# Kernel optimization log

Hardware: AMD Instinct MI355X
Metric: run time of the kernel (lower is better)

Reference implementation:

```python
import jax, jax.numpy as jnp
import numpy as np

N_HEAD, N_KV_HEAD, HEAD_DIM = 16, 4, 128
EPS = 1e-5


def rms_norm(x, eps=EPS):
    return x * jax.lax.rsqrt(jnp.mean(x * x, axis=-1, keepdims=True) + eps)


def apply_rope(x, cos, sin):
    # x: (B,T,H,D); cos/sin: (1,T,1,D//2)
    d = x.shape[-1] // 2
    x1, x2 = x[..., :d], x[..., d:]
    return jnp.concatenate([x1 * cos - x2 * sin, x1 * sin + x2 * cos], axis=-1)


def setup_inputs() -> dict:
    key = jax.random.key(0)
    ks = jax.random.split(key, 6)
    B, T, C = 4, 2048, 2048
    H, KV, D = N_HEAD, N_KV_HEAD, HEAD_DIM
    x = jax.random.normal(ks[0], (B, T, C), dtype=jnp.float32)
    # RoPE tables (llama-style, theta=10000)
    inv_freq = 1.0 / (10000.0 ** (jnp.arange(D // 2, dtype=jnp.float32) / (D // 2)))
    ang = jnp.arange(T, dtype=jnp.float32)[:, None] * inv_freq[None, :]  # (T, D/2)
    cos = jnp.cos(ang)[None, :, None, :]
    sin = jnp.sin(ang)[None, :, None, :]
    s = 0.02
    wq = jax.random.normal(ks[1], (C, H * D), dtype=jnp.float32) * s
    wk = jax.random.normal(ks[2], (C, KV * D), dtype=jnp.float32) * s
    wv = jax.random.normal(ks[3], (C, KV * D), dtype=jnp.float32) * s
    wproj = jax.random.normal(ks[4], (H * D, C), dtype=jnp.float32) * s
    return {"x": x, "cos": cos, "sin": sin, "wq": wq, "wk": wk, "wv": wv, "wproj": wproj}


def reference(x, cos, sin, wq, wk, wv, wproj):
    B, T, C = x.shape
    H, KV, D = N_HEAD, N_KV_HEAD, HEAD_DIM
    n_rep = H // KV
    q = (x @ wq).reshape(B, T, H, D)
    k = (x @ wk).reshape(B, T, KV, D)
    v = (x @ wv).reshape(B, T, KV, D)
    q = apply_rope(q, cos, sin)
    k = apply_rope(k, cos, sin)
    # QK-norm (use_qk_norm=True)
    q = rms_norm(q)
    k = rms_norm(k)
    # GQA: expand kv heads (matches torch repeat_interleave on head dim)
    k = jnp.repeat(k, n_rep, axis=2)
    v = jnp.repeat(v, n_rep, axis=2)
    scale = 1.0 / np.sqrt(D).astype(np.float32)
    scores = jnp.einsum('bqhd,bkhd->bhqk', q, k) * scale  # (B,H,T,T)
    causal = jnp.tril(jnp.ones((T, T), dtype=bool))
    scores = jnp.where(causal[None, None], scores, jnp.finfo(scores.dtype).min)
    p = jax.nn.softmax(scores, axis=-1)
    y = jnp.einsum('bhqk,bkhd->bqhd', p, v).reshape(B, T, H * D)
    return y @ wproj
```

## Files before the change

kernel.cpp:

```cpp
#include <hip/hip_runtime.h>
#include <hip/hip_bf16.h>
#include <stdint.h>

using bf16 = __hip_bfloat16;
typedef __attribute__((ext_vector_type(8))) short short8;
typedef __attribute__((ext_vector_type(4))) float f32x4;
typedef __attribute__((ext_vector_type(16))) float f32x16;

#define MFMA16(a,b,c) __builtin_amdgcn_mfma_f32_16x16x32_bf16(a,b,c,0,0,0)
#define MFMA32(a,b,c) __builtin_amdgcn_mfma_f32_32x32x16_bf16(a,b,c,0,0,0)

__device__ __forceinline__ void gload_lds16(const void* g, void* l) {
  __builtin_amdgcn_global_load_lds((const __attribute__((address_space(1))) void*)g,
                                   (__attribute__((address_space(3))) void*)l, 16, 0, 0);
}

__device__ __forceinline__ short bf_bits(float f) {
  bf16 h = __float2bfloat16(f);
  return *reinterpret_cast<short*>(&h);
}
__device__ __forceinline__ unsigned int pk2(float a, float b) {
  unsigned int r;
  asm("v_cvt_pk_bf16_f32 %0, %1, %2" : "=v"(r) : "v"(a), "v"(b));
  return r;
}
__device__ __forceinline__ float bf2f(short s) {
  return __uint_as_float((unsigned int)(unsigned short)s << 16);
}
__device__ __forceinline__ float exp2g(float x) { return __builtin_amdgcn_exp2f(x); }

__global__ __launch_bounds__(256) void f32_to_bf16_k(const float* __restrict__ in,
                                                     bf16* __restrict__ out, size_t n) {
  size_t i = ((size_t)blockIdx.x * 256 + threadIdx.x) * 8;
  if (i >= n) return;
  float4 a = *(const float4*)(in + i);
  float4 b = *(const float4*)(in + i + 4);
  short8 pk;
  pk[0] = bf_bits(a.x); pk[1] = bf_bits(a.y); pk[2] = bf_bits(a.z); pk[3] = bf_bits(a.w);
  pk[4] = bf_bits(b.x); pk[5] = bf_bits(b.y); pk[6] = bf_bits(b.z); pk[7] = bf_bits(b.w);
  *(short8*)(out + i) = pk;
}

__global__ __launch_bounds__(256) void transpose_cvt_k(const float* __restrict__ in,
                                                       bf16* __restrict__ out, int K, int N) {
  __shared__ float tile[32][33];
  int n0 = blockIdx.x * 32, k0 = blockIdx.y * 32;
  int tx = threadIdx.x & 31, ty = threadIdx.x >> 5;
#pragma unroll
  for (int j = 0; j < 4; ++j) {
    int kk = ty + j * 8;
    tile[kk][tx] = in[(size_t)(k0 + kk) * N + n0 + tx];
  }
  __syncthreads();
#pragma unroll
  for (int j = 0; j < 4; ++j) {
    int nn = ty + j * 8;
    out[(size_t)(n0 + nn) * K + k0 + tx] = __float2bfloat16(tile[tx][nn]);
  }
}

__global__ __launch_bounds__(256) void transpose_v_k(const bf16* __restrict__ qkv,
                                                     bf16* __restrict__ vt) {
  constexpr int T = 2048, Dh = 128, KV = 4, QKVW = 3072, VOFF = 2560;
  __shared__ bf16 tile[32][33];
  int t0 = blockIdx.x * 32, d0 = blockIdx.y * 32;
  int b = blockIdx.z >> 2, kv = blockIdx.z & 3;
  int tx = threadIdx.x & 31, ty = threadIdx.x >> 5;
#pragma unroll
  for (int j = 0; j < 4; ++j) {
    int tt = ty + j * 8;
    tile[tt][tx] = qkv[((size_t)(b * T + t0 + tt)) * QKVW + VOFF + kv * Dh + d0 + tx];
  }
  __syncthreads();
#pragma unroll
  for (int j = 0; j < 4; ++j) {
    int dd = ty + j * 8;
    vt[((size_t)((b * KV + kv) * Dh + d0 + dd)) * T + t0 + tx] = tile[tx][dd];
  }
}

__global__ __launch_bounds__(256) void rope_rms_k(bf16* __restrict__ buf, int rowstride,
                                                  int baseoff,
                                                  const float* __restrict__ cosp,
                                                  const float* __restrict__ sinp,
                                                  int nh, float outscale) {
  constexpr int T = 2048;
  int wid = blockIdx.x * 4 + (threadIdx.x >> 6);
  int lane = threadIdx.x & 63;
  int h = wid % nh;
  int tok = wid / nh;
  int t = tok & (T - 1);
  bf16* p = buf + (size_t)tok * rowstride + baseoff + h * 128;
  float x1 = __bfloat162float(p[lane]);
  float x2 = __bfloat162float(p[lane + 64]);
  float c = cosp[t * 64 + lane], s = sinp[t * 64 + lane];
  float o1 = x1 * c - x2 * s;
  float o2 = x1 * s + x2 * c;
  float ss = o1 * o1 + o2 * o2;
#pragma unroll
  for (int m = 1; m < 64; m <<= 1) ss += __shfl_xor(ss, m, 64);
  float r = rsqrtf(ss * (1.f / 128.f) + 1e-5f) * outscale;
  p[lane] = __float2bfloat16(o1 * r);
  p[lane + 64] = __float2bfloat16(o2 * r);
}

#define PHASE(buf, i0, ...)                                                       \
  {                                                                               \
    short8 a00 = ldA(buf, i0, 0), a01 = ldA(buf, i0, 1);                          \
    short8 a10 = ldA(buf, (i0) + 1, 0), a11 = ldA(buf, (i0) + 1, 1);              \
    __VA_ARGS__;                                                                  \
    __builtin_amdgcn_s_barrier();                                                 \
    asm volatile("s_waitcnt lgkmcnt(0)" ::: "memory");                            \
    __builtin_amdgcn_s_setprio(1);                                                \
    _Pragma("unroll") for (int j = 0; j < 4; ++j) {                               \
      acc[i0][j] = MFMA16(a00, bf_[2 * j], acc[i0][j]);                           \
      acc[i0][j] = MFMA16(a01, bf_[2 * j + 1], acc[i0][j]);                       \
      acc[(i0) + 1][j] = MFMA16(a10, bf_[2 * j], acc[(i0) + 1][j]);               \
      acc[(i0) + 1][j] = MFMA16(a11, bf_[2 * j + 1], acc[(i0) + 1][j]);           \
    }                                                                             \
    __builtin_amdgcn_s_setprio(0);                                                \
  }
#define LOADB(buf)                                                                \
  _Pragma("unroll") for (int j = 0; j < 4; ++j) {                                 \
    bf_[2 * j] = ldB(buf, j, 0);                                                  \
    bf_[2 * j + 1] = ldB(buf, j, 1);                                              \
  }
#define BAR __builtin_amdgcn_s_barrier()

template <typename OutT>
__global__ __launch_bounds__(512, 2) void gemm256(const bf16* __restrict__ A,
                                                  const bf16* __restrict__ Bt,
                                                  OutT* __restrict__ C, int K,
                                                  int NT, int ldC) {
  __shared__ char lds[131072];
  const int tid = threadIdx.x, lane = tid & 63, w = tid >> 6;
  const int wm = w >> 2, wn = w & 3;
  const int bx = blockIdx.x;
  const int chunk = gridDim.x >> 3;
  const int wgid = (bx & 7) * chunk + (bx >> 3);
  const int m0 = (wgid / NT) * 256, n0 = (wgid % NT) * 256;
  const int lm = lane & 15;
  const int sw = (lane & 7) << 4;
  const int g16 = (lane >> 4) << 4;
  const size_t strideAB = (size_t)K * 2;

  auto stageA = [&](int buf, int h, int t) {
#pragma unroll
    for (int p2 = 0; p2 < 2; ++p2) {
      int off = tid * 16 + p2 * 8192;
      int row = off >> 7, cb = off & 127;
      int scb = cb ^ ((row & 7) << 4);
      gload_lds16((const char*)A + (size_t)(m0 + h * 128 + row) * strideAB + t * 128 + scb,
                  lds + buf * 65536 + h * 16384 + off);
    }
  };
  auto stageB = [&](int buf, int h, int t) {
#pragma unroll
    for (int p2 = 0; p2 < 2; ++p2) {
      int off = tid * 16 + p2 * 8192;
      int row = off >> 7, cb = off & 127;
      int scb = cb ^ ((row & 7) << 4);
      gload_lds16((const char*)Bt + (size_t)(n0 + h * 128 + row) * strideAB + t * 128 + scb,
                  lds + buf * 65536 + 32768 + h * 16384 + off);
    }
  };
  auto ldA = [&](int buf, int i, int ks) {
    int row = wm * 128 + i * 16 + lm;
    return *(const short8*)(lds + buf * 65536 + row * 128 + ((ks * 64 + g16) ^ sw));
  };
  auto ldB = [&](int buf, int j, int ks) {
    int row = wn * 64 + j * 16 + lm;
    return *(const short8*)(lds + buf * 65536 + 32768 + row * 128 + ((ks * 64 + g16) ^ sw));
  };

  f32x4 acc[8][4] = {};
  short8 bf_[8];
  const int niter = K / 128;

  stageA(0, 0, 0); stageA(0, 1, 0); stageB(0, 0, 0); stageB(0, 1, 0);
  stageB(1, 0, 1); stageB(1, 1, 1);
  asm volatile("s_waitcnt vmcnt(4)" ::: "memory");
  BAR;

  for (int i = 0; i < niter; ++i) {
    const int t0 = 2 * i, t1 = 2 * i + 1;
    const bool nl = (i + 1 < niter);
    LOADB(0);
    PHASE(0, 0, stageA(1, 0, t1)); BAR;
    PHASE(0, 2, stageA(1, 1, t1)); BAR;
    PHASE(0, 4, if (nl) stageB(0, 0, t0 + 2)); BAR;
    PHASE(0, 6, if (nl) stageB(0, 1, t0 + 2));
    if (nl) { asm volatile("s_waitcnt vmcnt(4)" ::: "memory"); }
    else    { asm volatile("s_waitcnt vmcnt(0)" ::: "memory"); }
    BAR;
    LOADB(1);
    PHASE(1, 0, if (nl) stageA(0, 0, t0 + 2)); BAR;
    PHASE(1, 2, if (nl) stageA(0, 1, t0 + 2)); BAR;
    PHASE(1, 4, if (nl) stageB(1, 0, t1 + 2)); BAR;
    PHASE(1, 6, if (nl) stageB(1, 1, t1 + 2));
    if (nl) { asm volatile("s_waitcnt vmcnt(4)" ::: "memory"); }
    BAR;
  }

  if constexpr (sizeof(OutT) == 2) {
    __syncthreads();
    bf16* sC = (bf16*)lds;
#pragma unroll
    for (int i = 0; i < 8; ++i) {
      int row = wm * 128 + i * 16 + (lane >> 4) * 4;
#pragma unroll
      for (int j = 0; j < 4; ++j) {
        int col = wn * 64 + j * 16 + lm;
#pragma unroll
        for (int r = 0; r < 4; ++r) sC[(row + r) * 256 + col] = __float2bfloat16(acc[i][j][r]);
      }
    }
    __syncthreads();
#pragma unroll
    for (int p = 0; p < 16; ++p) {
      int off = tid * 16 + p * 8192;
      int row = off >> 9, cb = off & 511;
      *(short8*)((char*)C + ((size_t)(m0 + row) * ldC + n0) * 2 + cb) =
          *(const short8*)(lds + off);
    }
  } else {
#pragma unroll
    for (int i = 0; i < 8; ++i) {
      int row = m0 + wm * 128 + i * 16 + (lane >> 4) * 4;
#pragma unroll
      for (int j = 0; j < 4; ++j) {
        int col = n0 + wn * 64 + j * 16 + lm;
#pragma unroll
        for (int r = 0; r < 4; ++r) C[(size_t)(row + r) * ldC + col] = acc[i][j][r];
      }
    }
  }
}

template <typename OutT>
__global__ __launch_bounds__(256) void gemm_bt(const bf16* __restrict__ A,
                                               const bf16* __restrict__ Bt,
                                               OutT* __restrict__ C, int K,
                                               int NT, int ldC) {
  constexpr int BM = 128, BN = 128, BK = 64;
  __shared__ char smem[32768];
  bf16* sA = (bf16*)smem;
  bf16* sB = (bf16*)(smem + 16384);
  int tid = threadIdx.x;
  int lane = tid & 63, w = tid >> 6;
  int flat = blockIdx.x;
  int wgid = (flat & 7) * (gridDim.x >> 3) + (flat >> 3);
  int m0 = (wgid / NT) * BM, n0 = (wgid % NT) * BN;
  int wm = (w >> 1) * 64, wn = (w & 1) * 64;
  f32x4 acc[4][4] = {};
  int nk = K / BK;
  for (int kt = 0; kt < nk; ++kt) {
    __syncthreads();
    int kb = kt * BK;
#pragma unroll
    for (int it = 0; it < 4; ++it) {
      int off = tid * 16 + it * 4096;
      int row = off >> 7, cb = off & 127;
      gload_lds16((const char*)A + (((size_t)(m0 + row)) * K + kb) * 2 + cb, (char*)sA + off);
    }
#pragma unroll
    for (int it = 0; it < 4; ++it) {
      int off = tid * 16 + it * 4096;
      int row = off >> 7, cb = off & 127;
      gload_lds16((const char*)Bt + (((size_t)(n0 + row)) * K + kb) * 2 + cb, (char*)sB + off);
    }
    asm volatile("s_waitcnt vmcnt(0)" ::: "memory");
    __syncthreads();
#pragma unroll
    for (int ks = 0; ks < 2; ++ks) {
      short8 af[4], bfr[4];
#pragma unroll
      for (int i = 0; i < 4; ++i) {
        af[i]  = *(const short8*)(sA + (wm + i * 16 + (lane & 15)) * BK + ks * 32 + (lane >> 4) * 8);
        bfr[i] = *(const short8*)(sB + (wn + i * 16 + (lane & 15)) * BK + ks * 32 + (lane >> 4) * 8);
      }
#pragma unroll
      for (int i = 0; i < 4; ++i)
#pragma unroll
        for (int j = 0; j < 4; ++j)
          acc[i][j] = MFMA16(af[i], bfr[j], acc[i][j]);
    }
  }
  if constexpr (sizeof(OutT) == 2) {
    __syncthreads();
    bf16* sC = (bf16*)smem;
#pragma unroll
    for (int i = 0; i < 4; ++i) {
      int row = wm + i * 16 + (lane >> 4) * 4;
#pragma unroll
      for (int j = 0; j < 4; ++j) {
        int col = wn + j * 16 + (lane & 15);
#pragma unroll
        for (int r = 0; r < 4; ++r)
          sC[(row + r) * BN + col] = __float2bfloat16(acc[i][j][r]);
      }
    }
    __syncthreads();
#pragma unroll
    for (int it = 0; it < 8; ++it) {
      int off = tid * 16 + it * 4096;
      int row = off >> 8, cb = off & 255;
      *(short8*)((char*)C + ((size_t)(m0 + row) * ldC + n0) * 2 + cb) =
          *(const short8*)(smem + off);
    }
  } else {
#pragma unroll
    for (int i = 0; i < 4; ++i) {
      int row = m0 + wm + i * 16 + (lane >> 4) * 4;
#pragma unroll
      for (int j = 0; j < 4; ++j) {
        int col = n0 + wn + j * 16 + (lane & 15);
#pragma unroll
        for (int r = 0; r < 4; ++r)
          C[(size_t)(row + r) * ldC + col] = acc[i][j][r];
      }
    }
  }
}

__global__ __launch_bounds__(512, 2) void attn_k(const bf16* __restrict__ qkv,
                                                 const bf16* __restrict__ vt,
                                                 bf16* __restrict__ y,
                                                 const float* __restrict__ cosp,
                                                 const float* __restrict__ sinp) {
  constexpr int T = 2048, Dh = 128, KV = 4, KB = 64, QKVW = 3072, KOFF = 2048;
  __shared__ char lds[65536];
  const int tid = threadIdx.x, lane = tid & 63, w = tid >> 6;
  const int hi = lane >> 5, lq = lane & 31;
  const int bx = blockIdx.x;
  const int idx = (bx >> 6) & 3;
  const int qt = (bx < 256) ? (7 - idx) : idx;
  const int b = (bx >> 4) & 3, h = bx & 15;
  const int kh = h >> 2;
  const int q0 = qt * 256 + w * 32;
  const int qg = q0 + lq;
  const int swz = (lane & 7) << 4;

  short8 aq[8];
  {
    const bf16* qp = qkv + ((size_t)(b * T + qg)) * QKVW + h * Dh + hi * 8;
#pragma unroll
    for (int m = 0; m < 8; ++m) aq[m] = *(const short8*)(qp + m * 16);
  }
  __builtin_amdgcn_s_waitcnt(0);

  {
    float ss = 0.f;
#pragma unroll
    for (int m = 0; m < 8; ++m)
#pragma unroll
      for (int e = 0; e < 8; ++e) { float v = bf2f(aq[m][e]); ss += v * v; }
    ss += __shfl_xor(ss, 32, 64);
    float rn = rsqrtf(ss * (1.f / 128.f) + 1e-5f) * (0.08838834764831845f * 1.4426950408889634f);
    const float4* cq4 = (const float4*)(cosp + (size_t)qg * 64) + hi * 2;
    const float4* sq4 = (const float4*)(sinp + (size_t)qg * 64) + hi * 2;
#pragma unroll
    for (int m = 0; m < 4; ++m) {
      float4 c0 = cq4[m * 4], c1 = cq4[m * 4 + 1];
      float4 s0 = sq4[m * 4], s1 = sq4[m * 4 + 1];
      float cc[8] = {c0.x, c0.y, c0.z, c0.w, c1.x, c1.y, c1.z, c1.w};
      float sn[8] = {s0.x, s0.y, s0.z, s0.w, s1.x, s1.y, s1.z, s1.w};
      short8 xl = aq[m], xh = aq[m + 4], nl, nh;
#pragma unroll
      for (int e = 0; e < 8; ++e) {
        float x1 = bf2f(xl[e]), x2 = bf2f(xh[e]);
        nl[e] = bf_bits((x1 * cc[e] - x2 * sn[e]) * rn);
        nh[e] = bf_bits((x1 * sn[e] + x2 * cc[e]) * rn);
      }
      aq[m] = nl; aq[m + 4] = nh;
    }
  }

  f32x16 acc[4] = {};
  float mrow = -1e4f, lrow = 0.f;

  auto stage = [&](int buf, int kv0) {
#pragma unroll
    for (int p = 0; p < 2; ++p) {
      int off = tid * 16 + p * 8192;
      int row = off >> 8, cb = off & 255;
      int scb = cb ^ ((row & 7) << 4);
      gload_lds16((const char*)qkv + (((size_t)(b * T + kv0 + row)) * QKVW + KOFF + kh * Dh) * 2 + scb,
                  lds + buf * 16384 + off);
    }
#pragma unroll
    for (int p = 0; p < 2; ++p) {
      int off = tid * 16 + p * 8192;
      int row = off >> 7, cb = off & 127;
      int scb = cb ^ ((row & 7) << 4);
      gload_lds16((const char*)vt + (((size_t)((b * KV + kh) * Dh + row)) * T + kv0) * 2 + scb,
                  lds + 32768 + buf * 16384 + off);
    }
  };

  const int nt = (qt + 1) * 4;
  const int lastit = (q0 + 31) >> 6;
  stage(0, 0);

  for (int it = 0; it < nt; ++it) {
    int cur = it & 1;
    if (it + 1 < nt) { stage(cur ^ 1, (it + 1) * KB); asm volatile("s_waitcnt vmcnt(4)" ::: "memory"); }
    else             { asm volatile("s_waitcnt vmcnt(0)" ::: "memory"); }
    __builtin_amdgcn_s_barrier();
    if (it <= lastit) {
      const char* sK = lds + cur * 16384;
      const char* sV = lds + 32768 + cur * 16384;
      const int kv0 = it * KB;

      f32x16 s0 = {}, s1 = {};
      __builtin_amdgcn_s_setprio(1);
#pragma unroll
      for (int m = 0; m < 8; ++m) {
        short8 ak = *(const short8*)(sK + lq * 256 + ((m * 32 + hi * 16) ^ swz));
        s0 = MFMA32(ak, aq[m], s0);
      }
#pragma unroll
      for (int m = 0; m < 8; ++m) {
        short8 ak = *(const short8*)(sK + (32 + lq) * 256 + ((m * 32 + hi * 16) ^ swz));
        s1 = MFMA32(ak, aq[m], s1);
      }
      __builtin_amdgcn_s_setprio(0);

      if (kv0 + 63 > q0) {
#pragma unroll
        for (int r = 0; r < 16; ++r) {
          int krow = (r & 3) + 8 * (r >> 2) + 4 * hi;
          if (kv0 + krow > qg) s0[r] = -1e30f;
          if (kv0 + 32 + krow > qg) s1[r] = -1e30f;
        }
      }

      float mx[16];
#pragma unroll
      for (int r = 0; r < 16; ++r) mx[r] = fmaxf(s0[r], s1[r]);
#pragma unroll
      for (int st = 8; st > 0; st >>= 1)
#pragma unroll
        for (int r = 0; r < 16; ++r) if (r < st) mx[r] = fmaxf(mx[r], mx[r + st]);
      float tmax = fmaxf(mx[0], __shfl_xor(mx[0], 32, 64));
      if (!__all(tmax - mrow <= 11.5f)) {
        float mn = fmaxf(mrow, tmax);
        float corr = exp2g(mrow - mn);
        mrow = mn;
        lrow *= corr;
#pragma unroll
        for (int dt = 0; dt < 4; ++dt)
#pragma unroll
          for (int r = 0; r < 16; ++r) acc[dt][r] *= corr;
      }
      float sm[16];
#pragma unroll
      for (int r = 0; r < 16; ++r) {
        s0[r] = exp2g(s0[r] - mrow);
        s1[r] = exp2g(s1[r] - mrow);
        sm[r] = s0[r] + s1[r];
      }
#pragma unroll
      for (int st = 8; st > 0; st >>= 1)
#pragma unroll
        for (int r = 0; r < 16; ++r) if (r < st) sm[r] += sm[r + st];
      lrow += sm[0] + __shfl_xor(sm[0], 32, 64);

      unsigned int u[16];
#pragma unroll
      for (int g = 0; g < 4; ++g) {
        u[g * 2 + 0] = pk2(s0[4 * g + 0], s0[4 * g + 1]);
        u[g * 2 + 1] = pk2(s0[4 * g + 2], s0[4 * g + 3]);
        u[8 + g * 2 + 0] = pk2(s1[4 * g + 0], s1[4 * g + 1]);
        u[8 + g * 2 + 1] = pk2(s1[4 * g + 2], s1[4 * g + 3]);
      }
      short8 pb[4];
#pragma unroll
      for (int kvs = 0; kvs < 4; ++kvs) {
        unsigned int lo0 = u[4 * kvs + 0], lo1 = u[4 * kvs + 1];
        unsigned int hi0 = u[4 * kvs + 2], hi1 = u[4 * kvs + 3];
        asm volatile("v_permlane32_swap_b32 %0, %1" : "+v"(lo0), "+v"(hi0));
        asm volatile("v_permlane32_swap_b32 %0, %1" : "+v"(lo1), "+v"(hi1));
        union { short8 v; unsigned int q[4]; } P;
        P.q[0] = lo0; P.q[1] = lo1; P.q[2] = hi0; P.q[3] = hi1;
        pb[kvs] = P.v;
      }

      __builtin_amdgcn_s_setprio(1);
#pragma unroll
      for (int dt = 0; dt < 4; ++dt) {
#pragma unroll
        for (int kvs = 0; kvs < 4; ++kvs) {
          short8 av = *(const short8*)(sV + (dt * 32 + lq) * 128 + ((kvs * 32 + hi * 16) ^ swz));
          acc[dt] = MFMA32(av, pb[kvs], acc[dt]);
        }
      }
      __builtin_amdgcn_s_setprio(0);
    }
    __builtin_amdgcn_s_barrier();
  }

  float inv = 1.f / lrow;
  __syncthreads();
  char* myO = lds + w * 8192;
#pragma unroll
  for (int dt = 0; dt < 4; ++dt)
#pragma unroll
    for (int i = 0; i < 8; ++i) {
      int d = ((2 * i) & 3) + 8 * (i >> 1) + 4 * hi;
      unsigned int pkd = pk2(acc[dt][2 * i] * inv, acc[dt][2 * i + 1] * inv);
      *(unsigned int*)(myO + lq * 256 + ((dt * 64 + d * 2) ^ ((lq & 7) << 4))) = pkd;
    }
  __syncthreads();
  const int row0 = b * T + qt * 256;
#pragma unroll
  for (int p = 0; p < 8; ++p) {
    int off = (p * 512 + tid) * 16;
    int q = off >> 8, cb = off & 255;
    short8 v = *(const short8*)(lds + (q >> 5) * 8192 + (q & 31) * 256 + (cb ^ ((q & 7) << 4)));
    *(short8*)((char*)y + ((size_t)(row0 + q) * 2048 + h * 128) * 2 + cb) = v;
  }
}

extern "C" void kernel_launch(void* const* d_in, const int* in_sizes, int n_in,
                              void* d_out, int out_size, void* d_ws, size_t ws_size,
                              hipStream_t stream) {
  const float* x    = (const float*)d_in[0];
  const float* cosp = (const float*)d_in[1];
  const float* sinp = (const float*)d_in[2];
  const float* wq   = (const float*)d_in[3];
  const float* wk   = (const float*)d_in[4];
  const float* wv   = (const float*)d_in[5];
  const float* wp   = (const float*)d_in[6];
  float* out = (float*)d_out;

  constexpr size_t Mtok = 8192;
  constexpr int Cdim = 2048, HD = 2048, KVD = 512, QKVW = 3072;

  char* ws = (char*)d_ws;
  bf16* xb    = (bf16*)ws; ws += Mtok * Cdim * 2;
  bf16* wqkvT = (bf16*)ws; ws += (size_t)QKVW * Cdim * 2;
  bf16* wpT   = (bf16*)ws; ws += (size_t)Cdim * HD * 2;
  bf16* qkv   = (bf16*)ws; ws += Mtok * QKVW * 2;
  bf16* vtb   = (bf16*)ws; ws += Mtok * KVD * 2;
  bf16* yb    = (bf16*)ws; ws += Mtok * HD * 2;

  f32_to_bf16_k<<<dim3(Mtok * Cdim / 8 / 256), 256, 0, stream>>>(x, xb, Mtok * Cdim);
  transpose_cvt_k<<<dim3(HD / 32, Cdim / 32), 256, 0, stream>>>(wq, wqkvT, Cdim, HD);
  transpose_cvt_k<<<dim3(KVD / 32, Cdim / 32), 256, 0, stream>>>(wk, wqkvT + (size_t)2048 * Cdim, Cdim, KVD);
  transpose_cvt_k<<<dim3(KVD / 32, Cdim / 32), 256, 0, stream>>>(wv, wqkvT + (size_t)2560 * Cdim, Cdim, KVD);
  transpose_cvt_k<<<dim3(Cdim / 32, HD / 32), 256, 0, stream>>>(wp, wpT, HD, Cdim);

  gemm256<bf16><<<dim3(256), 512, 0, stream>>>(xb, wqkvT, qkv, Cdim, 8, QKVW);
  gemm_bt<bf16><<<dim3(512), 256, 0, stream>>>(xb, wqkvT + (size_t)2048 * Cdim,
                                               (bf16*)qkv + 2048, Cdim, 8, QKVW);

  rope_rms_k<<<dim3(Mtok * 4 / 4), 256, 0, stream>>>(qkv, QKVW, 2048, cosp, sinp, 4, 1.0f);
  transpose_v_k<<<dim3(64, 4, 16), 256, 0, stream>>>(qkv, vtb);

  attn_k<<<dim3(512), 512, 0, stream>>>(qkv, vtb, yb, cosp, sinp);

  gemm256<float><<<dim3(256), 512, 0, stream>>>(yb, wpT, out, Cdim, 8, 2048);
}
```

Baseline: 333.7 us.

## Pair complementary causal query tiles per attention block to share K/V loads

Each attention block now processes two query tiles, qt and 7-qt, so the causal work per block is balanced. Both tiles consume the same staged K/V tiles from LDS, which halves K/V global traffic for the smaller tile. The grid is halved to 256 blocks. In exchange, register pressure doubles (two Q fragments and two accumulators per wave), which risks spills or lower occupancy under launch_bounds(512,2), and the grid now fills fewer CUs.

```diff
diff --git a/kernel.cpp b/kernel.cpp
--- a/kernel.cpp
+++ b/kernel.cpp
@@ -333,23 +333,24 @@
   const int tid = threadIdx.x, lane = tid & 63, w = tid >> 6;
   const int hi = lane >> 5, lq = lane & 31;
   const int bx = blockIdx.x;
-  const int idx = (bx >> 6) & 3;
-  const int qt = (bx < 256) ? (7 - idx) : idx;
+  const int pidx = bx >> 6;
+  const int qtA = 7 - pidx, qtB = pidx;
   const int b = (bx >> 4) & 3, h = bx & 15;
   const int kh = h >> 2;
-  const int q0 = qt * 256 + w * 32;
-  const int qg = q0 + lq;
+  const int q0A = qtA * 256 + w * 32, qgA = q0A + lq;
+  const int q0B = qtB * 256 + w * 32, qgB = q0B + lq;
   const int swz = (lane & 7) << 4;
 
-  short8 aq[8];
+  short8 aqA[8], aqB[8];
   {
-    const bf16* qp = qkv + ((size_t)(b * T + qg)) * QKVW + h * Dh + hi * 8;
-#pragma unroll
-    for (int m = 0; m < 8; ++m) aq[m] = *(const short8*)(qp + m * 16);
+    const bf16* qpA = qkv + ((size_t)(b * T + qgA)) * QKVW + h * Dh + hi * 8;
+    const bf16* qpB = qkv + ((size_t)(b * T + qgB)) * QKVW + h * Dh + hi * 8;
+#pragma unroll
+    for (int m = 0; m < 8; ++m) { aqA[m] = *(const short8*)(qpA + m * 16); aqB[m] = *(const short8*)(qpB + m * 16); }
   }
   __builtin_amdgcn_s_waitcnt(0);
 
-  {
+  auto ropeRms = [&](short8 (&aq)[8], int qg) {
     float ss = 0.f;
 #pragma unroll
     for (int m = 0; m < 8; ++m)
@@ -374,10 +375,12 @@
       }
       aq[m] = nl; aq[m + 4] = nh;
     }
-  }
-
-  f32x16 acc[4] = {};
-  float mrow = -1e4f, lrow = 0.f;
+  };
+  ropeRms(aqA, qgA);
+  ropeRms(aqB, qgB);
+
+  f32x16 accA[4] = {}, accB[4] = {};
+  float mrowA = -1e4f, lrowA = 0.f, mrowB = -1e4f, lrowB = 0.f;
 
   auto stage = [&](int buf, int kv0) {
 #pragma unroll
@@ -398,128 +401,136 @@
     }
   };
 
-  const int nt = (qt + 1) * 4;
-  const int lastit = (q0 + 31) >> 6;
+  auto process = [&](short8 (&aq)[8], f32x16 (&acc)[4], float& mrow, float& lrow,
+                     int q0l, int qgl, int kv0, const char* sK, const char* sV) {
+    f32x16 s0 = {}, s1 = {};
+    __builtin_amdgcn_s_setprio(1);
+#pragma unroll
+    for (int m = 0; m < 8; ++m) {
+      short8 ak = *(const short8*)(sK + lq * 256 + ((m * 32 + hi * 16) ^ swz));
+      s0 = MFMA32(ak, aq[m], s0);
+    }
+#pragma unroll
+    for (int m = 0; m < 8; ++m) {
+      short8 ak = *(const short8*)(sK + (32 + lq) * 256 + ((m * 32 + hi * 16) ^ swz));
+      s1 = MFMA32(ak, aq[m], s1);
+    }
+    __builtin_amdgcn_s_setprio(0);
+
+    if (kv0 + 63 > q0l) {
+#pragma unroll
+      for (int r = 0; r < 16; ++r) {
+        int krow = (r & 3) + 8 * (r >> 2) + 4 * hi;
+        if (kv0 + krow > qgl) s0[r] = -1e30f;
+        if (kv0 + 32 + krow > qgl) s1[r] = -1e30f;
+      }
+    }
+
+    float mx[16];
+#pragma unroll
+    for (int r = 0; r < 16; ++r) mx[r] = fmaxf(s0[r], s1[r]);
+#pragma unroll
+    for (int st = 8; st > 0; st >>= 1)
+#pragma unroll
+      for (int r = 0; r < 16; ++r) if (r < st) mx[r] = fmaxf(mx[r], mx[r + st]);
+    float tmax = fmaxf(mx[0], __shfl_xor(mx[0], 32, 64));
+    if (!__all(tmax - mrow <= 11.5f)) {
+      float mn = fmaxf(mrow, tmax);
+      float corr = exp2g(mrow - mn);
+      mrow = mn;
+      lrow *= corr;
+#pragma unroll
+      for (int dt = 0; dt < 4; ++dt)
+#pragma unroll
+        for (int r = 0; r < 16; ++r) acc[dt][r] *= corr;
+    }
+    float sm[16];
+#pragma unroll
+    for (int r = 0; r < 16; ++r) {
+      s0[r] = exp2g(s0[r] - mrow);
+      s1[r] = exp2g(s1[r] - mrow);
+      sm[r] = s0[r] + s1[r];
+    }
+#pragma unroll
+    for (int st = 8; st > 0; st >>= 1)
+#pragma unroll
+      for (int r = 0; r < 16; ++r) if (r < st) sm[r] += sm[r + st];
+    lrow += sm[0] + __shfl_xor(sm[0], 32, 64);
+
+    unsigned int u[16];
+#pragma unroll
+    for (int g = 0; g < 4; ++g) {
+      u[g * 2 + 0] = pk2(s0[4 * g + 0], s0[4 * g + 1]);
+      u[g * 2 + 1] = pk2(s0[4 * g + 2], s0[4 * g + 3]);
+      u[8 + g * 2 + 0] = pk2(s1[4 * g + 0], s1[4 * g + 1]);
+      u[8 + g * 2 + 1] = pk2(s1[4 * g + 2], s1[4 * g + 3]);
+    }
+    short8 pb[4];
+#pragma unroll
+    for (int kvs = 0; kvs < 4; ++kvs) {
+      unsigned int lo0 = u[4 * kvs + 0], lo1 = u[4 * kvs + 1];
+      unsigned int hi0 = u[4 * kvs + 2], hi1 = u[4 * kvs + 3];
+      asm volatile("v_permlane32_swap_b32 %0, %1" : "+v"(lo0), "+v"(hi0));
+      asm volatile("v_permlane32_swap_b32 %0, %1" : "+v"(lo1), "+v"(hi1));
+      union { short8 v; unsigned int q[4]; } P;
+      P.q[0] = lo0; P.q[1] = lo1; P.q[2] = hi0; P.q[3] = hi1;
+      pb[kvs] = P.v;
+    }
+
+    __builtin_amdgcn_s_setprio(1);
+#pragma unroll
+    for (int dt = 0; dt < 4; ++dt) {
+#pragma unroll
+      for (int kvs = 0; kvs < 4; ++kvs) {
+        short8 av = *(const short8*)(sV + (dt * 32 + lq) * 128 + ((kvs * 32 + hi * 16) ^ swz));
+        acc[dt] = MFMA32(av, pb[kvs], acc[dt]);
+      }
+    }
+    __builtin_amdgcn_s_setprio(0);
+  };
+
+  const int ntA = (qtA + 1) * 4;
+  const int lastitA = (q0A + 31) >> 6;
+  const int lastitB = (q0B + 31) >> 6;
   stage(0, 0);
 
-  for (int it = 0; it < nt; ++it) {
+  for (int it = 0; it < ntA; ++it) {
     int cur = it & 1;
-    if (it + 1 < nt) { stage(cur ^ 1, (it + 1) * KB); asm volatile("s_waitcnt vmcnt(4)" ::: "memory"); }
-    else             { asm volatile("s_waitcnt vmcnt(0)" ::: "memory"); }
+    if (it + 1 < ntA) { stage(cur ^ 1, (it + 1) * KB); asm volatile("s_waitcnt vmcnt(4)" ::: "memory"); }
+    else              { asm volatile("s_waitcnt vmcnt(0)" ::: "memory"); }
     __builtin_amdgcn_s_barrier();
-    if (it <= lastit) {
-      const char* sK = lds + cur * 16384;
-      const char* sV = lds + 32768 + cur * 16384;
-      const int kv0 = it * KB;
-
-      f32x16 s0 = {}, s1 = {};
-      __builtin_amdgcn_s_setprio(1);
-#pragma unroll
-      for (int m = 0; m < 8; ++m) {
-        short8 ak = *(const short8*)(sK + lq * 256 + ((m * 32 + hi * 16) ^ swz));
-        s0 = MFMA32(ak, aq[m], s0);
-      }
-#pragma unroll
-      for (int m = 0; m < 8; ++m) {
-        short8 ak = *(const short8*)(sK + (32 + lq) * 256 + ((m * 32 + hi * 16) ^ swz));
-        s1 = MFMA32(ak, aq[m], s1);
-      }
-      __builtin_amdgcn_s_setprio(0);
-
-      if (kv0 + 63 > q0) {
-#pragma unroll
-        for (int r = 0; r < 16; ++r) {
-          int krow = (r & 3) + 8 * (r >> 2) + 4 * hi;
-          if (kv0 + krow > qg) s0[r] = -1e30f;
-          if (kv0 + 32 + krow > qg) s1[r] = -1e30f;
-        }
-      }
-
-      float mx[16];
-#pragma unroll
-      for (int r = 0; r < 16; ++r) mx[r] = fmaxf(s0[r], s1[r]);
-#pragma unroll
-      for (int st = 8; st > 0; st >>= 1)
-#pragma unroll
-        for (int r = 0; r < 16; ++r) if (r < st) mx[r] = fmaxf(mx[r], mx[r + st]);
-      float tmax = fmaxf(mx[0], __shfl_xor(mx[0], 32, 64));
-      if (!__all(tmax - mrow <= 11.5f)) {
-        float mn = fmaxf(mrow, tmax);
-        float corr = exp2g(mrow - mn);
-        mrow = mn;
-        lrow *= corr;
-#pragma unroll
-        for (int dt = 0; dt < 4; ++dt)
-#pragma unroll
-          for (int r = 0; r < 16; ++r) acc[dt][r] *= corr;
-      }
-      float sm[16];
-#pragma unroll
-      for (int r = 0; r < 16; ++r) {
-        s0[r] = exp2g(s0[r] - mrow);
-        s1[r] = exp2g(s1[r] - mrow);
-        sm[r] = s0[r] + s1[r];
-      }
-#pragma unroll
-      for (int st = 8; st > 0; st >>= 1)
-#pragma unroll
-        for (int r = 0; r < 16; ++r) if (r < st) sm[r] += sm[r + st];
-      lrow += sm[0] + __shfl_xor(sm[0], 32, 64);
-
-      unsigned int u[16];
-#pragma unroll
-      for (int g = 0; g < 4; ++g) {
-        u[g * 2 + 0] = pk2(s0[4 * g + 0], s0[4 * g + 1]);
-        u[g * 2 + 1] = pk2(s0[4 * g + 2], s0[4 * g + 3]);
-        u[8 + g * 2 + 0] = pk2(s1[4 * g + 0], s1[4 * g + 1]);
-        u[8 + g * 2 + 1] = pk2(s1[4 * g + 2], s1[4 * g + 3]);
-      }
-      short8 pb[4];
-#pragma unroll
-      for (int kvs = 0; kvs < 4; ++kvs) {
-        unsigned int lo0 = u[4 * kvs + 0], lo1 = u[4 * kvs + 1];
-        unsigned int hi0 = u[4 * kvs + 2], hi1 = u[4 * kvs + 3];
-        asm volatile("v_permlane32_swap_b32 %0, %1" : "+v"(lo0), "+v"(hi0));
-        asm volatile("v_permlane32_swap_b32 %0, %1" : "+v"(lo1), "+v"(hi1));
-        union { short8 v; unsigned int q[4]; } P;
-        P.q[0] = lo0; P.q[1] = lo1; P.q[2] = hi0; P.q[3] = hi1;
-        pb[kvs] = P.v;
-      }
-
-      __builtin_amdgcn_s_setprio(1);
-#pragma unroll
-      for (int dt = 0; dt < 4; ++dt) {
-#pragma unroll
-        for (int kvs = 0; kvs < 4; ++kvs) {
-          short8 av = *(const short8*)(sV + (dt * 32 + lq) * 128 + ((kvs * 32 + hi * 16) ^ swz));
-          acc[dt] = MFMA32(av, pb[kvs], acc[dt]);
-        }
-      }
-      __builtin_amdgcn_s_setprio(0);
-    }
+    const char* sK = lds + cur * 16384;
+    const char* sV = lds + 32768 + cur * 16384;
+    const int kv0 = it * KB;
+    if (it <= lastitB) process(aqB, accB, mrowB, lrowB, q0B, qgB, kv0, sK, sV);
+    if (it <= lastitA) process(aqA, accA, mrowA, lrowA, q0A, qgA, kv0, sK, sV);
     __builtin_amdgcn_s_barrier();
   }
 
-  float inv = 1.f / lrow;
-  __syncthreads();
-  char* myO = lds + w * 8192;
-#pragma unroll
-  for (int dt = 0; dt < 4; ++dt)
-#pragma unroll
-    for (int i = 0; i < 8; ++i) {
-      int d = ((2 * i) & 3) + 8 * (i >> 1) + 4 * hi;
-      unsigned int pkd = pk2(acc[dt][2 * i] * inv, acc[dt][2 * i + 1] * inv);
-      *(unsigned int*)(myO + lq * 256 + ((dt * 64 + d * 2) ^ ((lq & 7) << 4))) = pkd;
-    }
-  __syncthreads();
-  const int row0 = b * T + qt * 256;
-#pragma unroll
-  for (int p = 0; p < 8; ++p) {
-    int off = (p * 512 + tid) * 16;
-    int q = off >> 8, cb = off & 255;
-    short8 v = *(const short8*)(lds + (q >> 5) * 8192 + (q & 31) * 256 + (cb ^ ((q & 7) << 4)));
-    *(short8*)((char*)y + ((size_t)(row0 + q) * 2048 + h * 128) * 2 + cb) = v;
-  }
+  auto writeOut = [&](f32x16 (&acc)[4], float lrow, int qt) {
+    float inv = 1.f / lrow;
+    __syncthreads();
+    char* myO = lds + w * 8192;
+#pragma unroll
+    for (int dt = 0; dt < 4; ++dt)
+#pragma unroll
+      for (int i = 0; i < 8; ++i) {
+        int d = ((2 * i) & 3) + 8 * (i >> 1) + 4 * hi;
+        unsigned int pkd = pk2(acc[dt][2 * i] * inv, acc[dt][2 * i + 1] * inv);
+        *(unsigned int*)(myO + lq * 256 + ((dt * 64 + d * 2) ^ ((lq & 7) << 4))) = pkd;
+      }
+    __syncthreads();
+    const int row0 = b * T + qt * 256;
+#pragma unroll
+    for (int p = 0; p < 8; ++p) {
+      int off = (p * 512 + tid) * 16;
+      int q = off >> 8, cb = off & 255;
+      short8 v = *(const short8*)(lds + (q >> 5) * 8192 + (q & 31) * 256 + (cb ^ ((q & 7) << 4)));
+      *(short8*)((char*)y + ((size_t)(row0 + q) * 2048 + h * 128) * 2 + cb) = v;
+    }
+  };
+  writeOut(accA, lrowA, qtA);
+  writeOut(accB, lrowB, qtB);
 }
 
 extern "C" void kernel_launch(void* const* d_in, const int* in_sizes, int n_in,
@@ -558,7 +569,7 @@
   rope_rms_k<<<dim3(Mtok * 4 / 4), 256, 0, stream>>>(qkv, QKVW, 2048, cosp, sinp, 4, 1.0f);
   transpose_v_k<<<dim3(64, 4, 16), 256, 0, stream>>>(qkv, vtb);
 
-  attn_k<<<dim3(512), 512, 0, stream>>>(qkv, vtb, yb, cosp, sinp);
+  attn_k<<<dim3(256), 512, 0, stream>>>(qkv, vtb, yb, cosp, sinp);
 
   gemm256<float><<<dim3(256), 512, 0, stream>>>(yb, wpT, out, Cdim, 8, 2048);
 }
```

Result: slower. 370.0 us (+10.9%).
